# Performance work log

Measured on AMD Instinct MI355X. Metric: run time of the kernel, lower is better.

The kernel has to match this reference:

```python
import jax, jax.numpy as jnp
import numpy as np

HIDDEN = 450
DEPTH = 8
VOCAB = 780
N_NODES = 5120
N_MESS = 10241


def setup_inputs() -> dict:
    key = jax.random.key(0)
    ks = jax.random.split(key, 16)
    s = 0.05  # weight scale for numerical sanity
    return {
        "fnode": jax.random.randint(ks[0], (N_NODES,), 0, VOCAB),
        "fmess": jax.random.randint(ks[1], (N_MESS,), 0, N_NODES),
        "node_graph": jax.random.randint(ks[2], (N_NODES, 6), 0, N_MESS),
        "mess_graph": jax.random.randint(ks[3], (N_MESS, 5), 0, N_MESS),
        "emb": jax.random.normal(ks[4], (VOCAB, HIDDEN), jnp.float32),
        "Wz": jax.random.normal(ks[5], (2 * HIDDEN, HIDDEN), jnp.float32) * s,
        "bz": jnp.zeros((HIDDEN,), jnp.float32),
        "Wr": jax.random.normal(ks[6], (HIDDEN, HIDDEN), jnp.float32) * s,
        "Ur": jax.random.normal(ks[7], (HIDDEN, HIDDEN), jnp.float32) * s,
        "bu": jnp.zeros((HIDDEN,), jnp.float32),
        "Wh": jax.random.normal(ks[8], (2 * HIDDEN, HIDDEN), jnp.float32) * s,
        "bh": jnp.zeros((HIDDEN,), jnp.float32),
        "Wo": jax.random.normal(ks[9], (2 * HIDDEN, HIDDEN), jnp.float32) * s,
        "bo": jnp.zeros((HIDDEN,), jnp.float32),
        "batch_size": 128,
    }


def _gru(fmess_e, mess_graph, Wz, bz, Wr, Ur, bu, Wh, bh):
    # JTNN graph-GRU: depth-unrolled message updates over the message graph.
    M = fmess_e.shape[0]
    h0 = jnp.zeros((M, HIDDEN), fmess_e.dtype)
    mask = jnp.ones((M, 1), fmess_e.dtype).at[0].set(0.0)  # slot 0 = dummy message
    r1 = (fmess_e @ Wr)[:, None, :]  # loop-invariant W_r(fmess), [M,1,H]

    def step(h, _):
        h_nei = h[mess_graph]                     # [M,K,H] gather (index_select_ND)
        sum_h = h_nei.sum(axis=1)                 # [M,H]
        z = jax.nn.sigmoid(jnp.concatenate([fmess_e, sum_h], -1) @ Wz + bz)
        r = jax.nn.sigmoid(r1 + h_nei @ Ur + bu)  # [M,K,H]
        sum_gh = (r * h_nei).sum(axis=1)
        pre_h = jnp.tanh(jnp.concatenate([fmess_e, sum_gh], -1) @ Wh + bh)
        h = ((1.0 - z) * sum_h + z * pre_h) * mask
        return h, None

    h, _ = jax.lax.scan(step, h0, None, length=DEPTH)
    return h


def reference(fnode, fmess, node_graph, mess_graph, emb, Wz, bz, Wr, Ur, bu,
              Wh, bh, Wo, bo, batch_size):
    x = emb[fnode]                    # [N,H] embedding gather
    fmess_e = x[fmess]                # [M,H] message input features
    h = _gru(fmess_e, mess_graph, Wz, bz, Wr, Ur, bu, Wh, bh)  # [M,H]
    mess_nei = h[node_graph]          # [N,Kn,H]
    node_vecs = jnp.concatenate([x, mess_nei.sum(axis=1)], -1)  # [N,2H]
    node_vecs = jax.nn.relu(node_vecs @ Wo + bo)                # outputNN
    # uniform scope: every tree has N_NODES // batch_size nodes -> static reshape
    tree_vecs = node_vecs.reshape(batch_size, -1, HIDDEN)       # [B,L,H]
    messages = jnp.zeros((mess_graph.shape[0], HIDDEN), node_vecs.dtype)
    return (tree_vecs, messages)
```

## Files before the change

### kernel.cpp

```cpp
#include <hip/hip_runtime.h>
#include <cstdint>
#include <cstddef>

#define H 450
#define H2 900
#define KP 480
#define KP2 960
#define NMESS 10241
#define NNODE 5120
#define MPAD 10368
#define SPP1 960
#define SPP2 1920
#define PPSZ ((size_t)MPAD * SPP1)
#define KM 5
#define KN 6
#define LDCH 960

typedef __attribute__((ext_vector_type(8))) short short8;
typedef __attribute__((ext_vector_type(4))) float f32x4;

__device__ __forceinline__ short bf16rne(float f) {
  union { float f; unsigned u; } x; x.f = f;
  unsigned u = x.u;
  u += 0x7FFF + ((u >> 16) & 1);
  return (short)(u >> 16);
}
__device__ __forceinline__ float bf16tof(short s) {
  union { float f; unsigned u; } x;
  x.u = ((unsigned)(unsigned short)s) << 16;
  return x.f;
}
__device__ __forceinline__ void bf16split(float v, short& hi, short& lo) {
  hi = bf16rne(v);
  lo = bf16rne(v - bf16tof(hi));
}
__device__ __forceinline__ float sigmoidf_(float x) {
  return 1.f / (1.f + __expf(-x));
}

__device__ __forceinline__ size_t ppix(int row, int k, int spp) {
  return (size_t)row * spp + ((k >> 5) << 6) + (k & 31);
}

__device__ __forceinline__ void gll16(const short* g, short* l) {
  __builtin_amdgcn_global_load_lds(
      (const __attribute__((address_space(1))) void*)g,
      (__attribute__((address_space(3))) void*)l, 16, 0, 0);
}

#define BM 64
#define BN 64
#define BK 32

struct SmemT { short As[2][64][64]; short Bs[2][64][64]; };

__device__ __forceinline__ void xcd_swz(int gx, int gy, int& bm, int& bn) {
  const int nwg = gx * gy;
  int lid = blockIdx.y * gx + blockIdx.x;
  const int q = nwg >> 3, r = nwg & 7;
  const int xcd = lid & 7, seq = lid >> 3;
  int sid = (xcd < r) ? (xcd * (q + 1) + seq)
                      : (r * (q + 1) + (xcd - r) * q + seq);
  bm = (sid / gx) * BM;
  bn = (sid % gx) * BN;
}

template<int ACT, int OUT>
__device__ __forceinline__ void gemm_core(
    SmemT& sm, const short* __restrict__ Apk, int Kpad,
    const short* __restrict__ Bpk,
    const float* __restrict__ bias,
    float* C, int ldc, short* Cs,
    int M, int N, int bm, int bn)
{
  const int tid  = threadIdx.x;
  const int lane = tid & 63;
  const int wid  = tid >> 6;
  const int wm   = (wid >> 1) * 32;
  const int wn   = (wid & 1) * 32;
  const int l15  = lane & 15;
  const int s8   = (lane >> 4) * 8;
  const int rr0  = (lane >> 4) * 4;
  const int spp  = Kpad * 2;

  const int lr = lane >> 3;
  const int sl = lane & 7;
  const int t0 = sl ^ lr;
  const short* src[4];
#pragma unroll
  for (int qq = 0; qq < 4; ++qq) {
    const int rrow = wid * 32 + qq * 8 + lr;
    const bool isA = rrow < 64;
    const int grow = isA ? (bm + rrow) : (bn + rrow - 64);
    src[qq] = (isA ? Apk : Bpk) + (size_t)grow * spp + t0 * 8;
  }
  const int nk = Kpad / BK;

  f32x4 acc[2][2];
#pragma unroll
  for (int i = 0; i < 2; ++i)
#pragma unroll
    for (int j = 0; j < 2; ++j)
#pragma unroll
      for (int t = 0; t < 4; ++t) acc[i][j][t] = 0.f;

  auto STAGE = [&](int b, int koff) {
#pragma unroll
    for (int qq = 0; qq < 4; ++qq) {
      const int r0 = wid * 32 + qq * 8;
      short* d = (r0 < 64) ? &sm.As[b][r0][0] : &sm.Bs[b][r0 - 64][0];
      gll16(src[qq] + koff, d);
    }
  };

  STAGE(0, 0);
  __syncthreads();
  int cur = 0;
  for (int t = 0; t < nk; ++t) {
    if (t + 1 < nk) STAGE(cur ^ 1, (t + 1) * 64);
    short8 ah[2], al[2], bh[2], bl[2];
#pragma unroll
    for (int i = 0; i < 2; ++i) {
      const int rA = wm + i*16 + l15;
      const int xr = (rA & 7) << 3;
      ah[i] = *(const short8*)&sm.As[cur][rA][(s8)      ^ xr];
      al[i] = *(const short8*)&sm.As[cur][rA][(s8 + 32) ^ xr];
    }
#pragma unroll
    for (int j = 0; j < 2; ++j) {
      const int rB = wn + j*16 + l15;
      const int xr = (rB & 7) << 3;
      bh[j] = *(const short8*)&sm.Bs[cur][rB][(s8)      ^ xr];
      bl[j] = *(const short8*)&sm.Bs[cur][rB][(s8 + 32) ^ xr];
    }
    __builtin_amdgcn_s_setprio(1);
#pragma unroll
    for (int j = 0; j < 2; ++j)
#pragma unroll
      for (int i = 0; i < 2; ++i) {
        acc[i][j] = __builtin_amdgcn_mfma_f32_16x16x32_bf16(ah[i], bh[j], acc[i][j], 0, 0, 0);
        acc[i][j] = __builtin_amdgcn_mfma_f32_16x16x32_bf16(al[i], bh[j], acc[i][j], 0, 0, 0);
        acc[i][j] = __builtin_amdgcn_mfma_f32_16x16x32_bf16(ah[i], bl[j], acc[i][j], 0, 0, 0);
      }
    __builtin_amdgcn_s_setprio(0);
    __syncthreads();
    cur ^= 1;
  }

#pragma unroll
  for (int j = 0; j < 2; ++j) {
    int col = bn + wn + j*16 + l15;
    if (col >= N) continue;
    float bv = bias ? bias[col] : 0.f;
#pragma unroll
    for (int i = 0; i < 2; ++i) {
      int row0 = bm + wm + i*16 + rr0;
#pragma unroll
      for (int rr = 0; rr < 4; ++rr) {
        int row = row0 + rr;
        if (row >= M) continue;
        float v = acc[i][j][rr] + bv;
        if (OUT == 0) {
          if (ACT == 1) v = fmaxf(v, 0.f);
          C[(size_t)row * ldc + col] = v;
        } else {
          Cs[(size_t)row * ldc + col] = bf16rne(v);
        }
      }
    }
  }
}

template<int ACT>
__global__ __launch_bounds__(256, 5)
void gemm4(const short* __restrict__ Apk, int Kpad,
           const short* __restrict__ Bpk,
           const float* __restrict__ bias,
           float* C, int ldc, int M, int N)
{
  __shared__ SmemT sm;
  int bm, bn; xcd_swz(gridDim.x, gridDim.y, bm, bn);
  gemm_core<ACT, 0>(sm, Apk, Kpad, Bpk, bias, C, ldc, nullptr, M, N, bm, bn);
}

__global__ __launch_bounds__(256, 5)
void gemm4_b(const short* __restrict__ Apk, int Kpad,
             const short* __restrict__ Bpk,
             const float* __restrict__ bias,
             short* Cs, int ldcs, int M, int N)
{
  __shared__ SmemT sm;
  int bm, bn; xcd_swz(gridDim.x, gridDim.y, bm, bn);
  gemm_core<0, 3>(sm, Apk, Kpad, Bpk, bias, nullptr, ldcs, Cs, M, N, bm, bn);
}

__global__ __launch_bounds__(256)
void k_wT(const float* __restrict__ W, int Kreal,
          short* __restrict__ Bt, int Kpad, int rmax) {
  __shared__ float T[32][33];
  const int tx = threadIdx.x & 31;
  const int ty = threadIdx.x >> 5;
  const int k0 = blockIdx.x * 32;
  const int c0 = blockIdx.y * 32;
  const int spp = Kpad * 2;
#pragma unroll
  for (int i = 0; i < 4; ++i) {
    int k = k0 + ty + i*8, c = c0 + tx;
    T[ty + i*8][tx] = (k < Kreal && c < H) ? W[(size_t)k * H + c] : 0.f;
  }
  __syncthreads();
#pragma unroll
  for (int i = 0; i < 4; ++i) {
    int c = c0 + ty + i*8, k = k0 + tx;
    if (k < Kpad && c < rmax) {
      short hi, lo;
      bf16split(T[tx][ty + i*8], hi, lo);
      size_t o = ppix(c, k, spp);
      Bt[o] = hi; Bt[o + 32] = lo;
    }
  }
}

__global__ void k_biascat(const float* __restrict__ bz, const float* __restrict__ bh,
                          float* __restrict__ biasI) {
  int c = blockIdx.x * blockDim.x + threadIdx.x;
  if (c >= 900) return;
  biasI[c] = (c < 450) ? bz[c] : bh[c - 450];
}


__global__ void k_build_idx(const int* __restrict__ fnode,
                            const int* __restrict__ fmess,
                            int* __restrict__ idxM) {
  int m = blockIdx.x * blockDim.x + threadIdx.x;
  if (m < NMESS) idxM[m] = fnode[fmess[m]];
}

__global__ void k_embsplit(const float* __restrict__ emb,
                           const int* __restrict__ idxM,
                           short* __restrict__ eP) {
  int m = blockIdx.x, j = threadIdx.x * 2;
  if (j >= KP) return;
  size_t o = ppix(m, j, SPP1);
  if (j < H) {
    float2 v = *(const float2*)&emb[(size_t)idxM[m] * H + j];
    short2 h2, l2;
    bf16split(v.x, h2.x, l2.x); bf16split(v.y, h2.y, l2.y);
    *(short2*)&eP[o] = h2; *(short2*)&eP[o + 32] = l2;
  } else {
    short2 z2; z2.x = 0; z2.y = 0;
    *(short2*)&eP[o] = z2; *(short2*)&eP[o + 32] = z2;
  }
}

__global__ void k_h1(const short* __restrict__ CHb, short* __restrict__ hP) {
  int m = blockIdx.x, j = threadIdx.x * 2;
  if (j >= KP) return;
  size_t oP = ppix(m, j, SPP1);
  if (j < H) {
    size_t oc = (size_t)m * LDCH + j;
    short2 cz2 = *(const short2*)&CHb[oc];
    short2 ch2 = *(const short2*)&CHb[oc + 450];
    float v0 = sigmoidf_(bf16tof(cz2.x)) * tanhf(bf16tof(ch2.x));
    float v1 = sigmoidf_(bf16tof(cz2.y)) * tanhf(bf16tof(ch2.y));
    if (m == 0) { v0 = 0.f; v1 = 0.f; }
    short2 h2, l2;
    bf16split(v0, h2.x, l2.x); bf16split(v1, h2.y, l2.y);
    *(short2*)&hP[oP] = h2; *(short2*)&hP[oP + 32] = l2;
  } else {
    short2 z2; z2.x = 0; z2.y = 0;
    *(short2*)&hP[oP] = z2; *(short2*)&hP[oP + 32] = z2;
  }
}

__global__ void k_gather3(const short* __restrict__ hP,
                          const short* __restrict__ GU,
                          const short* __restrict__ r1b,
                          const int* __restrict__ mg,
                          short* __restrict__ shP, short* __restrict__ ghP,
                          short* __restrict__ tzb) {
  int m = blockIdx.x, j = threadIdx.x * 2;
  if (j >= KP) return;
  size_t o = ppix(m, j, SPP1);
  if (j >= H) {
    short2 z2; z2.x = 0; z2.y = 0;
    *(short2*)&shP[o] = z2; *(short2*)&shP[o + 32] = z2;
    *(short2*)&ghP[o] = z2; *(short2*)&ghP[o + 32] = z2;
    return;
  }
  const int* e = mg + (size_t)m * KM;
  short2 rb2 = *(const short2*)&r1b[(size_t)m * 480 + j];
  float rb0 = bf16tof(rb2.x), rb1 = bf16tof(rb2.y);
  float s0 = 0.f, s1 = 0.f, t0 = 0.f, t1 = 0.f, u0 = 0.f, u1 = 0.f;
#pragma unroll
  for (int k = 0; k < KM; ++k) {
    int ek = e[k];
    size_t oP = ppix(ek, j, SPP1);
    size_t oG = (size_t)ek * LDCH + j;
    short2 gv = *(const short2*)&GU[oG];
    short2 uv = *(const short2*)&GU[oG + 450];
    short2 ph = *(const short2*)&hP[oP];
    short2 pl = *(const short2*)&hP[oP + 32];
    float h0 = bf16tof(ph.x) + bf16tof(pl.x);
    float h1 = bf16tof(ph.y) + bf16tof(pl.y);
    s0 += h0;                                  s1 += h1;
    t0 += sigmoidf_(rb0 + bf16tof(gv.x)) * h0; t1 += sigmoidf_(rb1 + bf16tof(gv.y)) * h1;
    u0 += bf16tof(uv.x);                       u1 += bf16tof(uv.y);
  }
  short2 h2, l2;
  bf16split(s0, h2.x, l2.x); bf16split(s1, h2.y, l2.y);
  *(short2*)&shP[o] = h2; *(short2*)&shP[o + 32] = l2;
  bf16split(t0, h2.x, l2.x); bf16split(t1, h2.y, l2.y);
  *(short2*)&ghP[o] = h2; *(short2*)&ghP[o + 32] = l2;
  short2 tz2; tz2.x = bf16rne(u0); tz2.y = bf16rne(u1);
  *(short2*)&tzb[(size_t)m * 480 + j] = tz2;
}

__global__ void k_combine(const short* __restrict__ CHb,
                          const short* __restrict__ tzb,
                          const short* __restrict__ thb,
                          const short* __restrict__ shP,
                          short* hP) {
  int m = blockIdx.x, j = threadIdx.x * 2;
  if (j >= H) return;
  size_t oc = (size_t)m * LDCH + j;
  size_t oP = ppix(m, j, SPP1);
  short2 cz2 = *(const short2*)&CHb[oc];
  short2 ch2 = *(const short2*)&CHb[oc + 450];
  short2 tz2 = *(const short2*)&tzb[(size_t)m * 480 + j];
  short2 th2 = *(const short2*)&thb[(size_t)m * 480 + j];
  short2 smh = *(const short2*)&shP[oP];
  short2 sml = *(const short2*)&shP[oP + 32];
  float sm0 = bf16tof(smh.x) + bf16tof(sml.x);
  float sm1 = bf16tof(smh.y) + bf16tof(sml.y);
  float z0 = sigmoidf_(bf16tof(cz2.x) + bf16tof(tz2.x));
  float z1 = sigmoidf_(bf16tof(cz2.y) + bf16tof(tz2.y));
  float p0 = tanhf(bf16tof(ch2.x) + bf16tof(th2.x));
  float p1 = tanhf(bf16tof(ch2.y) + bf16tof(th2.y));
  float v0 = (1.f - z0) * sm0 + z0 * p0;
  float v1 = (1.f - z1) * sm1 + z1 * p1;
  if (m == 0) { v0 = 0.f; v1 = 0.f; }
  short2 h2, l2;
  bf16split(v0, h2.x, l2.x); bf16split(v1, h2.y, l2.y);
  *(short2*)&hP[oP] = h2; *(short2*)&hP[oP + 32] = l2;
}

__global__ void k_nodecat(const float* __restrict__ emb,
                          const int* __restrict__ fnode,
                          const short* __restrict__ hP,
                          const int* __restrict__ ng,
                          short* __restrict__ Apk) {
  int n = blockIdx.x, t = threadIdx.x, j = t * 2;
  if (j < H) {
    float2 v = *(const float2*)&emb[(size_t)fnode[n] * H + j];
    short2 h2, l2;
    bf16split(v.x, h2.x, l2.x); bf16split(v.y, h2.y, l2.y);
    size_t o = ppix(n, j, SPP2);
    *(short2*)&Apk[o] = h2; *(short2*)&Apk[o + 32] = l2;

    const int* e = ng + (size_t)n * KN;
    float s0 = 0.f, s1 = 0.f;
#pragma unroll
    for (int k = 0; k < KN; ++k) {
      size_t oP = ppix(e[k], j, SPP1);
      short2 ph = *(const short2*)&hP[oP];
      short2 pl = *(const short2*)&hP[oP + 32];
      s0 += bf16tof(ph.x) + bf16tof(pl.x);
      s1 += bf16tof(ph.y) + bf16tof(pl.y);
    }
    bf16split(s0, h2.x, l2.x); bf16split(s1, h2.y, l2.y);
    o = ppix(n, 450 + j, SPP2);
    *(short2*)&Apk[o] = h2; *(short2*)&Apk[o + 32] = l2;
  }
  if (t < 30) {
    int c = 900 + t * 2;
    short2 z2; z2.x = 0; z2.y = 0;
    size_t o = ppix(n, c, SPP2);
    *(short2*)&Apk[o] = z2; *(short2*)&Apk[o + 32] = z2;
  }
}


extern "C" void kernel_launch(void* const* d_in, const int* in_sizes, int n_in,
                              void* d_out, int out_size, void* d_ws, size_t ws_size,
                              hipStream_t stream) {
  (void)in_sizes; (void)n_in; (void)out_size; (void)ws_size;

  const int*   fnode      = (const int*)d_in[0];
  const int*   fmess      = (const int*)d_in[1];
  const int*   node_graph = (const int*)d_in[2];
  const int*   mess_graph = (const int*)d_in[3];
  const float* emb        = (const float*)d_in[4];
  const float* Wz         = (const float*)d_in[5];
  const float* bz         = (const float*)d_in[6];
  const float* Wr         = (const float*)d_in[7];
  const float* Ur         = (const float*)d_in[8];
  const float* bu         = (const float*)d_in[9];
  const float* Wh         = (const float*)d_in[10];
  const float* bh         = (const float*)d_in[11];
  const float* Wo         = (const float*)d_in[12];
  const float* bo         = (const float*)d_in[13];

  short* P   = (short*)d_ws;
  short* hP  = P;
  short* shP = P + 1 * PPSZ;
  short* ghP = P + 2 * PPSZ;
  short* CHb = P + 3 * PPSZ;
  short* GU  = CHb + (size_t)NMESS * LDCH;
  short* r1b = GU  + (size_t)NMESS * LDCH;
  short* tzb = r1b + (size_t)NMESS * 480;
  short* thb = tzb + (size_t)NMESS * 480;

  char*  scr  = (char*)d_out + (size_t)NNODE * H * 4;
  short* BtI  = (short*)scr;
  short* BtR  = BtI  + (size_t)1408 * SPP1;
  short* BtGU = BtR  + (size_t)512 * SPP1;
  short* BtHH = BtGU + (size_t)1024 * SPP1;
  short* BtO  = BtHH + (size_t)512 * SPP1;
  float* biasI = (float*)(BtO + (size_t)512 * SPP2);
  int*   idxM  = (int*)(biasI + 912);

  k_build_idx<<<(NMESS + 255) / 256, 256, 0, stream>>>(fnode, fmess, idxM);

  dim3 gT(KP / 32, 16), gT2(KP2 / 32, 16);
  k_wT<<<gT,  256, 0, stream>>>(Wz,                  H, BtI,               KP,  512);
  k_wT<<<gT,  256, 0, stream>>>(Wh,                  H, BtI + 450 * SPP1,  KP,  512);
  k_wT<<<gT,  256, 0, stream>>>(Wr,                  H, BtR,               KP,  512);
  k_wT<<<gT,  256, 0, stream>>>(Ur,                  H, BtGU,              KP,  512);
  k_wT<<<gT,  256, 0, stream>>>(Wz + (size_t)H * H,  H, BtGU + 450 * SPP1, KP,  512);
  k_wT<<<gT,  256, 0, stream>>>(Wh + (size_t)H * H,  H, BtHH,              KP,  512);
  k_wT<<<gT2, 256, 0, stream>>>(Wo,                 H2, BtO,               KP2, 512);
  k_biascat<<<4, 256, 0, stream>>>(bz, bh, biasI);

  k_embsplit<<<NMESS, 256, 0, stream>>>(emb, idxM, ghP);

  dim3 gI1(15, MPAD / BM);
  gemm4_b<<<gI1, 256, 0, stream>>>(ghP, KP, BtI, biasI, CHb, LDCH, NMESS, H2);
  dim3 gI2(8, MPAD / BM);
  gemm4_b<<<gI2, 256, 0, stream>>>(ghP, KP, BtR, bu, r1b, 480, NMESS, H);

  k_h1<<<NMESS, 256, 0, stream>>>(CHb, hP);

  dim3 gGU(15, MPAD / BM);
  dim3 gB(8, MPAD / BM);
  for (int d = 1; d < 8; ++d) {
    gemm4_b<<<gGU, 256, 0, stream>>>(hP, KP, BtGU, nullptr, GU, LDCH, NMESS, H2);
    k_gather3<<<NMESS, 256, 0, stream>>>(hP, GU, r1b, mess_graph, shP, ghP, tzb);
    gemm4_b<<<gB, 256, 0, stream>>>(ghP, KP, BtHH, nullptr, thb, 480, NMESS, H);
    k_combine<<<NMESS, 256, 0, stream>>>(CHb, tzb, thb, shP, hP);
  }

  k_nodecat<<<NNODE, 256, 0, stream>>>(emb, fnode, hP, node_graph, shP);
  dim3 gF(8, NNODE / BM);
  gemm4<1><<<gF, 256, 0, stream>>>(shP, KP2, BtO, bo, (float*)d_out, H, NNODE, H);

  hipMemsetAsync((float*)d_out + (size_t)NNODE * H, 0, (size_t)NMESS * H * sizeof(float), stream);
}
```

Measured before the change: 922.1 us.

## Apply Wz to summed neighbor state instead of summing projected neighbors

```diff
diff --git a/kernel.cpp b/kernel.cpp
--- a/kernel.cpp
+++ b/kernel.cpp
@@ -194,6 +194,20 @@
   gemm_core<0, 3>(sm, Apk, Kpad, Bpk, bias, nullptr, ldcs, Cs, M, N, bm, bn);
 }
 
+__global__ __launch_bounds__(256, 5)
+void gemm4_pair(const short* __restrict__ A0, const short* __restrict__ B0,
+                short* C0,
+                const short* __restrict__ A1, const short* __restrict__ B1,
+                short* C1)
+{
+  __shared__ SmemT sm;
+  int bm, bn; xcd_swz(gridDim.x, gridDim.y, bm, bn);
+  if (blockIdx.z == 0)
+    gemm_core<0, 3>(sm, A0, KP, B0, nullptr, nullptr, 480, C0, NMESS, H, bm, bn);
+  else
+    gemm_core<0, 3>(sm, A1, KP, B1, nullptr, nullptr, 480, C1, NMESS, H, bm, bn);
+}
+
 __global__ __launch_bounds__(256)
 void k_wT(const float* __restrict__ W, int Kreal,
           short* __restrict__ Bt, int Kpad, int rmax) {
@@ -273,12 +287,11 @@
   }
 }
 
-__global__ void k_gather3(const short* __restrict__ hP,
-                          const short* __restrict__ GU,
+__global__ void k_gather2(const short* __restrict__ hP,
+                          const short* __restrict__ gb,
                           const short* __restrict__ r1b,
                           const int* __restrict__ mg,
-                          short* __restrict__ shP, short* __restrict__ ghP,
-                          short* __restrict__ tzb) {
+                          short* __restrict__ shP, short* __restrict__ ghP) {
   int m = blockIdx.x, j = threadIdx.x * 2;
   if (j >= KP) return;
   size_t o = ppix(m, j, SPP1);
@@ -291,29 +304,24 @@
   const int* e = mg + (size_t)m * KM;
   short2 rb2 = *(const short2*)&r1b[(size_t)m * 480 + j];
   float rb0 = bf16tof(rb2.x), rb1 = bf16tof(rb2.y);
-  float s0 = 0.f, s1 = 0.f, t0 = 0.f, t1 = 0.f, u0 = 0.f, u1 = 0.f;
+  float s0 = 0.f, s1 = 0.f, t0 = 0.f, t1 = 0.f;
 #pragma unroll
   for (int k = 0; k < KM; ++k) {
     int ek = e[k];
     size_t oP = ppix(ek, j, SPP1);
-    size_t oG = (size_t)ek * LDCH + j;
-    short2 gv = *(const short2*)&GU[oG];
-    short2 uv = *(const short2*)&GU[oG + 450];
+    short2 gv = *(const short2*)&gb[(size_t)ek * 480 + j];
     short2 ph = *(const short2*)&hP[oP];
     short2 pl = *(const short2*)&hP[oP + 32];
     float h0 = bf16tof(ph.x) + bf16tof(pl.x);
     float h1 = bf16tof(ph.y) + bf16tof(pl.y);
     s0 += h0;                                  s1 += h1;
     t0 += sigmoidf_(rb0 + bf16tof(gv.x)) * h0; t1 += sigmoidf_(rb1 + bf16tof(gv.y)) * h1;
-    u0 += bf16tof(uv.x);                       u1 += bf16tof(uv.y);
   }
   short2 h2, l2;
   bf16split(s0, h2.x, l2.x); bf16split(s1, h2.y, l2.y);
   *(short2*)&shP[o] = h2; *(short2*)&shP[o + 32] = l2;
   bf16split(t0, h2.x, l2.x); bf16split(t1, h2.y, l2.y);
   *(short2*)&ghP[o] = h2; *(short2*)&ghP[o + 32] = l2;
-  short2 tz2; tz2.x = bf16rne(u0); tz2.y = bf16rne(u1);
-  *(short2*)&tzb[(size_t)m * 480 + j] = tz2;
 }
 
 __global__ void k_combine(const short* __restrict__ CHb,
@@ -406,16 +414,17 @@
   short* shP = P + 1 * PPSZ;
   short* ghP = P + 2 * PPSZ;
   short* CHb = P + 3 * PPSZ;
-  short* GU  = CHb + (size_t)NMESS * LDCH;
-  short* r1b = GU  + (size_t)NMESS * LDCH;
+  short* gb  = CHb + (size_t)NMESS * LDCH;
+  short* r1b = gb  + (size_t)NMESS * 480;
   short* tzb = r1b + (size_t)NMESS * 480;
   short* thb = tzb + (size_t)NMESS * 480;
 
   char*  scr  = (char*)d_out + (size_t)NNODE * H * 4;
   short* BtI  = (short*)scr;
   short* BtR  = BtI  + (size_t)1408 * SPP1;
-  short* BtGU = BtR  + (size_t)512 * SPP1;
-  short* BtHH = BtGU + (size_t)1024 * SPP1;
+  short* BtUr = BtR  + (size_t)512 * SPP1;
+  short* BtZ  = BtUr + (size_t)512 * SPP1;
+  short* BtHH = BtZ  + (size_t)512 * SPP1;
   short* BtO  = BtHH + (size_t)512 * SPP1;
   float* biasI = (float*)(BtO + (size_t)512 * SPP2);
   int*   idxM  = (int*)(biasI + 912);
@@ -426,8 +435,8 @@
   k_wT<<<gT,  256, 0, stream>>>(Wz,                  H, BtI,               KP,  512);
   k_wT<<<gT,  256, 0, stream>>>(Wh,                  H, BtI + 450 * SPP1,  KP,  512);
   k_wT<<<gT,  256, 0, stream>>>(Wr,                  H, BtR,               KP,  512);
-  k_wT<<<gT,  256, 0, stream>>>(Ur,                  H, BtGU,              KP,  512);
-  k_wT<<<gT,  256, 0, stream>>>(Wz + (size_t)H * H,  H, BtGU + 450 * SPP1, KP,  512);
+  k_wT<<<gT,  256, 0, stream>>>(Ur,                  H, BtUr,              KP,  512);
+  k_wT<<<gT,  256, 0, stream>>>(Wz + (size_t)H * H,  H, BtZ,               KP,  512);
   k_wT<<<gT,  256, 0, stream>>>(Wh + (size_t)H * H,  H, BtHH,              KP,  512);
   k_wT<<<gT2, 256, 0, stream>>>(Wo,                 H2, BtO,               KP2, 512);
   k_biascat<<<4, 256, 0, stream>>>(bz, bh, biasI);
@@ -441,12 +450,12 @@
 
   k_h1<<<NMESS, 256, 0, stream>>>(CHb, hP);
 
-  dim3 gGU(15, MPAD / BM);
   dim3 gB(8, MPAD / BM);
+  dim3 gP(8, MPAD / BM, 2);
   for (int d = 1; d < 8; ++d) {
-    gemm4_b<<<gGU, 256, 0, stream>>>(hP, KP, BtGU, nullptr, GU, LDCH, NMESS, H2);
-    k_gather3<<<NMESS, 256, 0, stream>>>(hP, GU, r1b, mess_graph, shP, ghP, tzb);
-    gemm4_b<<<gB, 256, 0, stream>>>(ghP, KP, BtHH, nullptr, thb, 480, NMESS, H);
+    gemm4_b<<<gB, 256, 0, stream>>>(hP, KP, BtUr, nullptr, gb, 480, NMESS, H);
+    k_gather2<<<NMESS, 256, 0, stream>>>(hP, gb, r1b, mess_graph, shP, ghP);
+    gemm4_pair<<<gP, 256, 0, stream>>>(ghP, BtHH, thb, shP, BtZ, tzb);
     k_combine<<<NMESS, 256, 0, stream>>>(CHb, tzb, thb, shP, hP);
   }
 
```

Result: faster. 827.6 us (-10.2%).
